# Performance work log

Measured on AMD Instinct MI355X. Metric: run time of the kernel, lower is better.

## Reference

```python
import jax, jax.numpy as jnp
import numpy as np

WS = 7    # window size
SS = 3    # shift size
NH = 6    # num heads
EPS = 1e-5


def _ln(x, g, b):
    m = jnp.mean(x, -1, keepdims=True)
    v = jnp.mean((x - m) ** 2, -1, keepdims=True)
    return (x - m) * jax.lax.rsqrt(v + EPS) * g + b


def _win_part(x, ws):
    # (B, H, W, C) -> (B*nW, ws*ws, C)
    B, H, W, C = x.shape
    x = x.reshape(B, H // ws, ws, W // ws, ws, C).transpose(0, 1, 3, 2, 4, 5)
    return x.reshape(-1, ws * ws, C)


def _win_rev(w, ws, B, H, W):
    # (B*nW, ws*ws, C) -> (B, H, W, C)
    C = w.shape[-1]
    x = w.reshape(B, H // ws, W // ws, ws, ws, C).transpose(0, 1, 3, 2, 4, 5)
    return x.reshape(B, H, W, C)


def _forward(x, norm1_g, norm1_b, qkv_w, qkv_b, proj_w, proj_b, norm2_g, norm2_b,
             fc1_w, fc1_b, fc2_w, fc2_b, rel_table, mask_matrix, H, W, rel_index):
    B, L, C = x.shape
    hd = C // NH
    shortcut = x
    h = _ln(x, norm1_g, norm1_b).reshape(B, H, W, C)
    pad_r = (WS - W % WS) % WS
    pad_b = (WS - H % WS) % WS
    h = jnp.pad(h, ((0, 0), (0, pad_b), (0, pad_r), (0, 0)))
    Hp, Wp = H + pad_b, W + pad_r
    # cyclic shift (shift_size > 0 path)
    h = jnp.roll(h, (-SS, -SS), axis=(1, 2))
    xw = _win_part(h, WS)                                   # [Bw, N, C]
    Bw, N, _ = xw.shape
    qkv = (xw @ qkv_w + qkv_b).reshape(Bw, N, 3, NH, hd)
    q = qkv[:, :, 0].transpose(0, 2, 1, 3) * (hd ** -0.5)   # [Bw, NH, N, hd]
    k = qkv[:, :, 1].transpose(0, 2, 1, 3)
    v = qkv[:, :, 2].transpose(0, 2, 1, 3)
    attn = q @ k.transpose(0, 1, 3, 2)                      # [Bw, NH, N, N]
    bias = rel_table[rel_index.reshape(-1)].reshape(N, N, NH).transpose(2, 0, 1)
    attn = attn + bias[None]
    nW = mask_matrix.shape[0]
    attn = attn.reshape(Bw // nW, nW, NH, N, N) + mask_matrix[None, :, None]
    attn = jax.nn.softmax(attn.reshape(Bw, NH, N, N), axis=-1)
    o = (attn @ v).transpose(0, 2, 1, 3).reshape(Bw, N, C)
    o = o @ proj_w + proj_b
    h = _win_rev(o, WS, B, Hp, Wp)
    h = jnp.roll(h, (SS, SS), axis=(1, 2))[:, :H, :W, :].reshape(B, L, C)
    x = shortcut + h
    y = _ln(x, norm2_g, norm2_b)
    y = jax.nn.gelu(y @ fc1_w + fc1_b, approximate=False) @ fc2_w + fc2_b  # torch GELU = exact erf
    return x + y


def setup_inputs() -> dict:
    B, H, W, C, HID = 32, 56, 56, 192, 768
    ws, ss = WS, SS
    ks = jax.random.split(jax.random.key(0), 8)
    rn = lambda i, shp, s: jax.random.normal(ks[i], shp, jnp.float32) * s
    inp = {
        'x': rn(0, (B, H * W, C), 1.0),
        'norm1_g': jnp.ones((C,), jnp.float32), 'norm1_b': jnp.zeros((C,), jnp.float32),
        'qkv_w': rn(1, (C, 3 * C), 0.02), 'qkv_b': jnp.zeros((3 * C,), jnp.float32),
        'proj_w': rn(2, (C, C), 0.02), 'proj_b': jnp.zeros((C,), jnp.float32),
        'norm2_g': jnp.ones((C,), jnp.float32), 'norm2_b': jnp.zeros((C,), jnp.float32),
        'fc1_w': rn(3, (C, HID), 0.02), 'fc1_b': jnp.zeros((HID,), jnp.float32),
        'fc2_w': rn(4, (HID, C), 0.02), 'fc2_b': jnp.zeros((C,), jnp.float32),
        'rel_table': rn(5, ((2 * ws - 1) ** 2, NH), 0.02),
    }
    # relative position index (same construction as torch buffer)
    coords = np.stack(np.meshgrid(np.arange(ws), np.arange(ws), indexing='ij')).reshape(2, -1)
    rel = (coords[:, :, None] - coords[:, None, :]).transpose(1, 2, 0)
    rel[..., 0] += ws - 1
    rel[..., 1] += ws - 1
    rel[..., 0] *= 2 * ws - 1
    inp['rel_index'] = jnp.asarray(rel.sum(-1), jnp.int32)  # [49, 49]
    # shifted-window attention mask (standard Swin construction)
    img = np.zeros((1, H, W, 1), np.float32)
    cnt = 0
    for hs in (slice(0, -ws), slice(-ws, -ss), slice(-ss, None)):
        for wsl in (slice(0, -ws), slice(-ws, -ss), slice(-ss, None)):
            img[:, hs, wsl, :] = cnt
            cnt += 1
    mw = img.reshape(1, H // ws, ws, W // ws, ws, 1).transpose(0, 1, 3, 2, 4, 5).reshape(-1, ws * ws)
    diff = mw[:, None, :] - mw[:, :, None]
    inp['mask_matrix'] = jnp.asarray(np.where(diff != 0, -100.0, 0.0), jnp.float32)  # [64, 49, 49]
    inp['H'] = H
    inp['W'] = W
    return inp


def reference(x, norm1_g, norm1_b, qkv_w, qkv_b, proj_w, proj_b, norm2_g, norm2_b,
              fc1_w, fc1_b, fc2_w, fc2_b, rel_table, rel_index, mask_matrix, H, W):
    return _forward(x, norm1_g, norm1_b, qkv_w, qkv_b, proj_w, proj_b, norm2_g, norm2_b,
                    fc1_w, fc1_b, fc2_w, fc2_b, rel_table, mask_matrix, H, W, rel_index)
```

## Files before the change

### kernel.cpp

```cpp
#include <hip/hip_runtime.h>

typedef __bf16 bf8 __attribute__((ext_vector_type(8)));
typedef float f4 __attribute__((ext_vector_type(4)));

__device__ __forceinline__ float b2f(unsigned short u) {
  union { unsigned int i; float f; } c; c.i = ((unsigned int)u) << 16; return c.f;
}
__device__ __forceinline__ unsigned short f2b(float f) {
  union { float f; unsigned int i; } c; c.f = f;
  unsigned int i = c.i;
  return (unsigned short)((i + 0x7FFFu + ((i >> 16) & 1u)) >> 16);
}

__global__ void transpose_kernel(const float* __restrict__ in,
                                 unsigned short* __restrict__ out, int K, int N) {
  int idx = blockIdx.x * 256 + threadIdx.x;
  if (idx < K * N) {
    int n = idx / K, k = idx - n * K;
    out[idx] = f2b(in[k * N + n]);
  }
}

__global__ __launch_bounds__(256) void ln_kernel(const float* __restrict__ xin,
                                                 const float* __restrict__ g,
                                                 const float* __restrict__ bb,
                                                 unsigned short* __restrict__ out) {
  long token = (long)blockIdx.x * 4 + (threadIdx.x >> 6);
  int lane = threadIdx.x & 63;
  const float* row = xin + token * 192;
  float v[3] = {row[lane], row[lane + 64], row[lane + 128]};
  float s = v[0] + v[1] + v[2];
#pragma unroll
  for (int m = 1; m < 64; m <<= 1) s += __shfl_xor(s, m, 64);
  float mean = s * (1.0f / 192.0f);
  float d0 = v[0] - mean, d1 = v[1] - mean, d2 = v[2] - mean;
  float dd = d0 * d0 + d1 * d1 + d2 * d2;
#pragma unroll
  for (int m = 1; m < 64; m <<= 1) dd += __shfl_xor(dd, m, 64);
  float rstd = rsqrtf(dd * (1.0f / 192.0f) + 1e-5f);
  unsigned short* orow = out + token * 192;
#pragma unroll
  for (int i = 0; i < 3; i++) {
    int c = lane + i * 64;
    orow[c] = f2b((v[i] - mean) * rstd * g[c] + bb[c]);
  }
}

template <int EPI>
__global__ __launch_bounds__(256) void gemm_kernel(const unsigned short* __restrict__ A,
                                                   const unsigned short* __restrict__ Bt,
                                                   const float* __restrict__ bias,
                                                   const float* __restrict__ res,
                                                   void* __restrict__ out, int K, int N) {
  __shared__ __align__(16) unsigned short As[64 * 32];
  __shared__ __align__(16) unsigned short Bs[64 * 32];
  const int tid = threadIdx.x;
  const int wave = tid >> 6;
  const int lane = tid & 63;
  const int quad = lane >> 4;
  const int l16 = lane & 15;
  const long m0 = (long)blockIdx.y * 64;
  const long n0 = (long)blockIdx.x * 64;

  const int sr = tid >> 2;
  const int sk = (tid & 3) * 8;
  const unsigned short* Ap = A + (m0 + sr) * K + sk;
  const unsigned short* Bp = Bt + (n0 + sr) * K + sk;

  f4 acc[4] = {};
  for (int k0 = 0; k0 < K; k0 += 32) {
    *(uint4*)&As[sr * 32 + sk] = *(const uint4*)(Ap + k0);
    *(uint4*)&Bs[sr * 32 + sk] = *(const uint4*)(Bp + k0);
    __syncthreads();
    bf8 a = *(const bf8*)&As[(wave * 16 + l16) * 32 + quad * 8];
#pragma unroll
    for (int nt = 0; nt < 4; nt++) {
      bf8 b = *(const bf8*)&Bs[(nt * 16 + l16) * 32 + quad * 8];
      acc[nt] = __builtin_amdgcn_mfma_f32_16x16x32_bf16(a, b, acc[nt], 0, 0, 0);
    }
    __syncthreads();
  }
#pragma unroll
  for (int nt = 0; nt < 4; nt++) {
    long n = n0 + nt * 16 + l16;
    float bv = bias[n];
#pragma unroll
    for (int r = 0; r < 4; r++) {
      long m = m0 + wave * 16 + quad * 4 + r;
      float v = acc[nt][r] + bv;
      long idx = m * N + n;
      if (EPI == 0) {
        ((unsigned short*)out)[idx] = f2b(v);
      } else if (EPI == 1) {
        ((float*)out)[idx] = v + res[idx];
      } else if (EPI == 2) {
        float gv = 0.5f * v * (1.0f + erff(v * 0.70710678118654752440f));
        ((unsigned short*)out)[idx] = f2b(gv);
      } else {
        ((float*)out)[idx] = v + res[idx];
      }
    }
  }
}

__global__ __launch_bounds__(128) void attn_kernel(const unsigned short* __restrict__ qkv,
                                                   const float* __restrict__ rel_t,
                                                   unsigned short* __restrict__ o) {
  __shared__ __align__(16) unsigned short sh[2 * 12032];
  __shared__ float relh[2][170];
  __shared__ int toksh[2][49];
  __shared__ int zsh[2][49];
  const int wave = threadIdx.x >> 6;
  const int lane = threadIdx.x & 63;
  const int quad = lane >> 4;
  const int l16 = lane & 15;
  const int p = blockIdx.x * 2 + wave;
  const int head = p % 6;
  const int wib = p / 6;
  const int wi = wib & 63;
  const int b = wib >> 6;
  unsigned short* Qs = sh + wave * 12032;
  unsigned short* Ks = Qs + 2560;
  unsigned short* Vts = Qs + 5120;
  unsigned short* Ps = Qs + 7424;

  if (lane < 49) {
    int r = lane / 7, c = lane - (lane / 7) * 7;
    int ph = (wi >> 3) * 7 + r, pw = (wi & 7) * 7 + c;
    int h = ph + 3; if (h >= 56) h -= 56;
    int w = pw + 3; if (w >= 56) w -= 56;
    toksh[wave][lane] = (b * 56 + h) * 56 + w;
    int zh = (ph < 49) ? 0 : (ph < 53 ? 1 : 2);
    int zw = (pw < 49) ? 0 : (pw < 53 ? 1 : 2);
    zsh[wave][lane] = zh * 3 + zw;
  }
  for (int i = lane; i < 169; i += 64) relh[wave][i] = rel_t[i * 6 + head];
  {
    unsigned int* qz = (unsigned int*)(Qs + 49 * 40);
    unsigned int* kz = (unsigned int*)(Ks + 49 * 40);
    for (int i = lane; i < 300; i += 64) { qz[i] = 0u; kz[i] = 0u; }
#pragma unroll
    for (int e = 0; e < 4; e++) {
      int ee = lane + e * 64;
      int d = ee >> 3, c8 = ee & 7;
      *(unsigned int*)&Vts[d * 72 + 48 + c8 * 2] = 0u;
    }
  }
  __syncthreads();

  for (int e = lane; e < 196; e += 64) {
    int n = e >> 2, c = e & 3;
    int t = toksh[wave][n];
    const uint4* src = (const uint4*)(qkv + (long)t * 576 + head * 32);
    uint4 qc = src[c];
    uint4 kc = src[c + 24];
    uint4 vc = src[c + 48];
    *(uint4*)&Qs[n * 40 + c * 8] = qc;
    *(uint4*)&Ks[n * 40 + c * 8] = kc;
    const unsigned short* vv = (const unsigned short*)&vc;
#pragma unroll
    for (int j = 0; j < 8; j++) Vts[(c * 8 + j) * 72 + n] = vv[j];
  }
  __syncthreads();

  bf8 af[4], bf_[4];
#pragma unroll
  for (int i = 0; i < 4; i++) af[i] = *(const bf8*)&Qs[(16 * i + l16) * 40 + quad * 8];
#pragma unroll
  for (int j = 0; j < 4; j++) bf_[j] = *(const bf8*)&Ks[(16 * j + l16) * 40 + quad * 8];
  f4 S[4][4];
#pragma unroll
  for (int i = 0; i < 4; i++)
#pragma unroll
    for (int j = 0; j < 4; j++)
      S[i][j] = __builtin_amdgcn_mfma_f32_16x16x32_bf16(af[i], bf_[j], (f4){0.f, 0.f, 0.f, 0.f}, 0, 0, 0);

  int colv[4], colkey[4], zcol[4];
#pragma unroll
  for (int jt = 0; jt < 4; jt++) {
    int col = 16 * jt + l16;
    int cc = col < 49 ? col : 48;
    int rj = cc / 7, cj = cc - rj * 7;
    colkey[jt] = rj * 13 + cj;
    zcol[jt] = zsh[wave][cc];
    colv[jt] = (col < 49);
  }

  const float sc = 0.17677669529663687f;
#pragma unroll
  for (int it = 0; it < 4; it++) {
#pragma unroll
    for (int r = 0; r < 4; r++) {
      int row = 16 * it + quad * 4 + r;
      int row2 = row < 49 ? row : 48;
      int ri = row2 / 7, ci = row2 - ri * 7;
      int rk = ri * 13 + ci + 84;
      int zr = zsh[wave][row2];
      float v[4];
#pragma unroll
      for (int jt = 0; jt < 4; jt++) {
        float bias = relh[wave][rk - colkey[jt]];
        float msk = (zr == zcol[jt]) ? 0.0f : -100.0f;
        float val = S[it][jt][r] * sc + bias + msk;
        v[jt] = colv[jt] ? val : -1e30f;
      }
      float mx = fmaxf(fmaxf(v[0], v[1]), fmaxf(v[2], v[3]));
#pragma unroll
      for (int m = 1; m < 16; m <<= 1) mx = fmaxf(mx, __shfl_xor(mx, m, 64));
      float e0 = __expf(v[0] - mx), e1 = __expf(v[1] - mx), e2 = __expf(v[2] - mx), e3 = __expf(v[3] - mx);
      float sum = e0 + e1 + e2 + e3;
#pragma unroll
      for (int m = 1; m < 16; m <<= 1) sum += __shfl_xor(sum, m, 64);
      float inv = 1.0f / sum;
      Ps[row * 72 + 0 + l16] = f2b(e0 * inv);
      Ps[row * 72 + 16 + l16] = f2b(e1 * inv);
      Ps[row * 72 + 32 + l16] = f2b(e2 * inv);
      Ps[row * 72 + 48 + l16] = f2b(e3 * inv);
    }
  }
  __syncthreads();

  f4 O[4][2] = {};
#pragma unroll
  for (int ks = 0; ks < 2; ks++) {
    bf8 pv[2];
#pragma unroll
    for (int nt = 0; nt < 2; nt++) pv[nt] = *(const bf8*)&Vts[(16 * nt + l16) * 72 + ks * 32 + quad * 8];
#pragma unroll
    for (int mt = 0; mt < 4; mt++) {
      bf8 pa = *(const bf8*)&Ps[(16 * mt + l16) * 72 + ks * 32 + quad * 8];
#pragma unroll
      for (int nt = 0; nt < 2; nt++)
        O[mt][nt] = __builtin_amdgcn_mfma_f32_16x16x32_bf16(pa, pv[nt], O[mt][nt], 0, 0, 0);
    }
  }
#pragma unroll
  for (int mt = 0; mt < 4; mt++) {
#pragma unroll
    for (int r = 0; r < 4; r++) {
      int row = 16 * mt + quad * 4 + r;
      if (row < 49) {
        long base = (long)toksh[wave][row] * 192 + head * 32 + l16;
        o[base] = f2b(O[mt][0][r]);
        o[base + 16] = f2b(O[mt][1][r]);
      }
    }
  }
}

extern "C" void kernel_launch(void* const* d_in, const int* in_sizes, int n_in,
                              void* d_out, int out_size, void* d_ws, size_t ws_size,
                              hipStream_t stream) {
  const float* x      = (const float*)d_in[0];
  const float* n1g    = (const float*)d_in[1];
  const float* n1b    = (const float*)d_in[2];
  const float* qkv_w  = (const float*)d_in[3];
  const float* qkv_b  = (const float*)d_in[4];
  const float* proj_w = (const float*)d_in[5];
  const float* proj_b = (const float*)d_in[6];
  const float* n2g    = (const float*)d_in[7];
  const float* n2b    = (const float*)d_in[8];
  const float* fc1_w  = (const float*)d_in[9];
  const float* fc1_b  = (const float*)d_in[10];
  const float* fc2_w  = (const float*)d_in[11];
  const float* fc2_b  = (const float*)d_in[12];
  const float* rel_t  = (const float*)d_in[13];
  const float* mask   = (const float*)d_in[15];
  (void)mask;

  char* ws = (char*)d_ws;
  unsigned short* qkv_wT  = (unsigned short*)(ws + 0);
  unsigned short* proj_wT = (unsigned short*)(ws + 221184);
  unsigned short* fc1_wT  = (unsigned short*)(ws + 294912);
  unsigned short* fc2_wT  = (unsigned short*)(ws + 589824);
  unsigned short* bufA    = (unsigned short*)(ws + 884736);
  unsigned short* bufB    = (unsigned short*)(ws + 39419904ULL);
  float*          xres    = (float*)(ws + 193560576ULL);

  const int M = 100352;

  transpose_kernel<<<(192 * 576 + 255) / 256, 256, 0, stream>>>(qkv_w, qkv_wT, 192, 576);
  transpose_kernel<<<(192 * 192 + 255) / 256, 256, 0, stream>>>(proj_w, proj_wT, 192, 192);
  transpose_kernel<<<(192 * 768 + 255) / 256, 256, 0, stream>>>(fc1_w, fc1_wT, 192, 768);
  transpose_kernel<<<(768 * 192 + 255) / 256, 256, 0, stream>>>(fc2_w, fc2_wT, 768, 192);

  ln_kernel<<<M / 4, 256, 0, stream>>>(x, n1g, n1b, bufA);
  gemm_kernel<0><<<dim3(576 / 64, M / 64), 256, 0, stream>>>(bufA, qkv_wT, qkv_b, nullptr, bufB, 192, 576);
  attn_kernel<<<12288 / 2, 128, 0, stream>>>(bufB, rel_t, bufA);
  gemm_kernel<1><<<dim3(192 / 64, M / 64), 256, 0, stream>>>(bufA, proj_wT, proj_b, x, xres, 192, 192);
  ln_kernel<<<M / 4, 256, 0, stream>>>(xres, n2g, n2b, bufA);
  gemm_kernel<2><<<dim3(768 / 64, M / 64), 256, 0, stream>>>(bufA, fc1_wT, fc1_b, nullptr, bufB, 192, 768);
  gemm_kernel<3><<<dim3(192 / 64, M / 64), 256, 0, stream>>>(bufB, fc2_wT, fc2_b, xres, d_out, 768, 192);
}
```

Baseline: 593.6 us.

## Rework GEMM with 128x64 tiles, double-buffered direct-to-LDS loads and XOR swizzle

```diff
diff --git a/kernel.cpp b/kernel.cpp
--- a/kernel.cpp
+++ b/kernel.cpp
@@ -10,6 +10,12 @@
   union { float f; unsigned int i; } c; c.f = f;
   unsigned int i = c.i;
   return (unsigned short)((i + 0x7FFFu + ((i >> 16) & 1u)) >> 16);
+}
+
+__device__ __forceinline__ void gl_lds16(const unsigned short* g, unsigned short* l) {
+  __builtin_amdgcn_global_load_lds((const __attribute__((address_space(1))) unsigned int*)g,
+                                   (__attribute__((address_space(3))) unsigned int*)l,
+                                   16, 0, 0);
 }
 
 __global__ void transpose_kernel(const float* __restrict__ in,
@@ -52,52 +58,99 @@
                                                    const float* __restrict__ bias,
                                                    const float* __restrict__ res,
                                                    void* __restrict__ out, int K, int N) {
-  __shared__ __align__(16) unsigned short As[64 * 32];
-  __shared__ __align__(16) unsigned short Bs[64 * 32];
+  __shared__ __align__(16) unsigned short As[2][128 * 64];
+  __shared__ __align__(16) unsigned short Bs[2][64 * 64];
   const int tid = threadIdx.x;
   const int wave = tid >> 6;
   const int lane = tid & 63;
   const int quad = lane >> 4;
   const int l16 = lane & 15;
-  const long m0 = (long)blockIdx.y * 64;
+  const long m0 = (long)blockIdx.y * 128;
   const long n0 = (long)blockIdx.x * 64;
 
-  const int sr = tid >> 2;
-  const int sk = (tid & 3) * 8;
-  const unsigned short* Ap = A + (m0 + sr) * K + sk;
-  const unsigned short* Bp = Bt + (n0 + sr) * K + sk;
-
-  f4 acc[4] = {};
-  for (int k0 = 0; k0 < K; k0 += 32) {
-    *(uint4*)&As[sr * 32 + sk] = *(const uint4*)(Ap + k0);
-    *(uint4*)&Bs[sr * 32 + sk] = *(const uint4*)(Bp + k0);
+  long a_src[4];
+  int a_dstc[4];
+#pragma unroll
+  for (int j = 0; j < 4; ++j) {
+    int L = (wave * 4 + j) * 64 + lane;
+    int row = L >> 3, cs = L & 7;
+    a_src[j] = (m0 + row) * (long)K + ((cs ^ (row & 7)) << 3);
+    a_dstc[j] = (wave * 4 + j) * 512;
+  }
+  long b_src[2];
+  int b_dstc[2];
+#pragma unroll
+  for (int j = 0; j < 2; ++j) {
+    int L = (wave * 2 + j) * 64 + lane;
+    int row = L >> 3, cs = L & 7;
+    b_src[j] = (n0 + row) * (long)K + ((cs ^ (row & 7)) << 3);
+    b_dstc[j] = (wave * 2 + j) * 512;
+  }
+
+  const int nT = K >> 6;
+  f4 acc[2][4] = {};
+
+#pragma unroll
+  for (int j = 0; j < 4; ++j) gl_lds16(A + a_src[j], &As[0][a_dstc[j]]);
+#pragma unroll
+  for (int j = 0; j < 2; ++j) gl_lds16(Bt + b_src[j], &Bs[0][b_dstc[j]]);
+
+  int cur = 0;
+  for (int t = 0; t < nT; ++t) {
+    if (t + 1 < nT) {
+      const int k0 = (t + 1) << 6;
+#pragma unroll
+      for (int j = 0; j < 4; ++j) gl_lds16(A + a_src[j] + k0, &As[cur ^ 1][a_dstc[j]]);
+#pragma unroll
+      for (int j = 0; j < 2; ++j) gl_lds16(Bt + b_src[j] + k0, &Bs[cur ^ 1][b_dstc[j]]);
+    }
     __syncthreads();
-    bf8 a = *(const bf8*)&As[(wave * 16 + l16) * 32 + quad * 8];
-#pragma unroll
-    for (int nt = 0; nt < 4; nt++) {
-      bf8 b = *(const bf8*)&Bs[(nt * 16 + l16) * 32 + quad * 8];
-      acc[nt] = __builtin_amdgcn_mfma_f32_16x16x32_bf16(a, b, acc[nt], 0, 0, 0);
+#pragma unroll
+    for (int kk = 0; kk < 2; ++kk) {
+      bf8 a[2], b[4];
+#pragma unroll
+      for (int mt = 0; mt < 2; ++mt) {
+        int r = wave * 32 + mt * 16 + l16;
+        int c = kk * 4 + quad;
+        a[mt] = *(const bf8*)&As[cur][r * 64 + ((c ^ (r & 7)) << 3)];
+      }
+#pragma unroll
+      for (int nt = 0; nt < 4; ++nt) {
+        int r = nt * 16 + l16;
+        int c = kk * 4 + quad;
+        b[nt] = *(const bf8*)&Bs[cur][r * 64 + ((c ^ (r & 7)) << 3)];
+      }
+#pragma unroll
+      for (int mt = 0; mt < 2; ++mt)
+#pragma unroll
+        for (int nt = 0; nt < 4; ++nt)
+          acc[mt][nt] = __builtin_amdgcn_mfma_f32_16x16x32_bf16(a[mt], b[nt], acc[mt][nt], 0, 0, 0);
     }
     __syncthreads();
-  }
-#pragma unroll
-  for (int nt = 0; nt < 4; nt++) {
+    cur ^= 1;
+  }
+
+#pragma unroll
+  for (int nt = 0; nt < 4; ++nt) {
     long n = n0 + nt * 16 + l16;
     float bv = bias[n];
 #pragma unroll
-    for (int r = 0; r < 4; r++) {
-      long m = m0 + wave * 16 + quad * 4 + r;
-      float v = acc[nt][r] + bv;
-      long idx = m * N + n;
-      if (EPI == 0) {
-        ((unsigned short*)out)[idx] = f2b(v);
-      } else if (EPI == 1) {
-        ((float*)out)[idx] = v + res[idx];
-      } else if (EPI == 2) {
-        float gv = 0.5f * v * (1.0f + erff(v * 0.70710678118654752440f));
-        ((unsigned short*)out)[idx] = f2b(gv);
-      } else {
-        ((float*)out)[idx] = v + res[idx];
+    for (int mt = 0; mt < 2; ++mt) {
+#pragma unroll
+      for (int r = 0; r < 4; ++r) {
+        long m = m0 + wave * 32 + mt * 16 + quad * 4 + r;
+        float v = acc[mt][nt][r] + bv;
+        long idx = m * N + n;
+        if (EPI == 0) {
+          ((unsigned short*)out)[idx] = f2b(v);
+        } else if (EPI == 1) {
+          ((float*)out)[idx] = v + res[idx];
+        } else if (EPI == 2) {
+          float gv = 0.5f * v * (1.0f + erff(v * 0.70710678118654752440f));
+          ((unsigned short*)out)[idx] = f2b(gv);
+        } else {
+          ((float*)out)[idx] = v + res[idx];
+        }
       }
     }
   }
@@ -285,10 +338,10 @@
   transpose_kernel<<<(768 * 192 + 255) / 256, 256, 0, stream>>>(fc2_w, fc2_wT, 768, 192);
 
   ln_kernel<<<M / 4, 256, 0, stream>>>(x, n1g, n1b, bufA);
-  gemm_kernel<0><<<dim3(576 / 64, M / 64), 256, 0, stream>>>(bufA, qkv_wT, qkv_b, nullptr, bufB, 192, 576);
+  gemm_kernel<0><<<dim3(576 / 64, M / 128), 256, 0, stream>>>(bufA, qkv_wT, qkv_b, nullptr, bufB, 192, 576);
   attn_kernel<<<12288 / 2, 128, 0, stream>>>(bufB, rel_t, bufA);
-  gemm_kernel<1><<<dim3(192 / 64, M / 64), 256, 0, stream>>>(bufA, proj_wT, proj_b, x, xres, 192, 192);
+  gemm_kernel<1><<<dim3(192 / 64, M / 128), 256, 0, stream>>>(bufA, proj_wT, proj_b, x, xres, 192, 192);
   ln_kernel<<<M / 4, 256, 0, stream>>>(xres, n2g, n2b, bufA);
-  gemm_kernel<2><<<dim3(768 / 64, M / 64), 256, 0, stream>>>(bufA, fc1_wT, fc1_b, nullptr, bufB, 192, 768);
-  gemm_kernel<3><<<dim3(192 / 64, M / 64), 256, 0, stream>>>(bufB, fc2_wT, fc2_b, xres, d_out, 768, 192);
-}
+  gemm_kernel<2><<<dim3(768 / 64, M / 128), 256, 0, stream>>>(bufA, fc1_wT, fc1_b, nullptr, bufB, 192, 768);
+  gemm_kernel<3><<<dim3(192 / 64, M / 128), 256, 0, stream>>>(bufB, fc2_wT, fc2_b, xres, d_out, 768, 192);
+}
```

Result: faster. 568.6 us (-4.2%).
